# Kernel optimization log

Hardware: AMD Instinct MI355X
Metric: run time of the kernel (lower is better)

Reference implementation:

```python
import jax, jax.numpy as jnp
import numpy as np


def dct2_mat(N):
    # Orthonormal DCT-II matrix M[k, n]; scipy dct(norm='ortho') == M @ x,
    # and since M is orthogonal, idct(norm='ortho') == M.T @ x.
    n = jnp.arange(N, dtype=jnp.float32)
    k = jnp.arange(N, dtype=jnp.float32)[:, None]
    M = jnp.cos(jnp.pi * (n + 0.5) * k / N)
    scale = jnp.where(k == 0, jnp.sqrt(1.0 / N), jnp.sqrt(2.0 / N))
    return (M * scale).astype(jnp.float32)


def setup_inputs() -> dict:
    key = jax.random.key(0)
    x = jax.random.normal(key, (8, 32, 64, 64, 64), dtype=jnp.float32)
    return {"x": x}


def reference(x):
    # Faithful to original: DCT is applied along B, D, H (axes 0,1,2 of the
    # permuted [B,D,H,W,C] tensor), crop/pad acts on D,H,W, then IDCT along B,D,H.
    OUT = (32, 32, 32)
    TR = (32, 32, 32)
    B, C, D, H, W = x.shape
    CB, CD, CH = dct2_mat(B), dct2_mat(D), dct2_mat(H)

    # forward DCT-II (ortho) along B, D, H as batched matmuls
    y = jnp.einsum('kb,bcdhw->kcdhw', CB, x)
    y = jnp.einsum('kd,bcdhw->bckhw', CD, y)
    y = jnp.einsum('kh,bcdhw->bcdkw', CH, y)

    # spectral crop along D, H, W, then zero-pad up to output_size
    y = y[:, :, :TR[0], :TR[1], :TR[2]]
    y = jnp.pad(y, ((0, 0), (0, 0),
                    (0, OUT[0] - TR[0]),
                    (0, OUT[1] - TR[1]),
                    (0, OUT[2] - TR[2])))

    # inverse DCT (ortho) = transpose of the (orthogonal) DCT matrix
    Bi, Di, Hi = y.shape[0], y.shape[2], y.shape[3]
    z = jnp.einsum('kn,kcdhw->ncdhw', dct2_mat(Bi), y)
    z = jnp.einsum('kn,bckhw->bcnhw', dct2_mat(Di), z)
    z = jnp.einsum('kn,bcdkw->bcdnw', dct2_mat(Hi), z)
    return z
```

## Files before the change

### kernel.cpp

```cpp
#include <hip/hip_runtime.h>


constexpr double kPI = 3.14159265358979323846;

constexpr double cos_poly(double x) {
  double r = 1.0;
  for (int k = 15; k >= 1; --k) r = 1.0 - r * x * x / ((2.0 * k) * (2.0 * k - 1.0));
  return r;
}
constexpr double csqrt(double v) {
  double r = (v > 1.0) ? v : 1.0;
  for (int i = 0; i < 64; ++i) r = 0.5 * (r + v / r);
  return r;
}

struct C64T  { double c[128]; };
struct C128T { double c[256]; };
constexpr C64T make_c64() {
  C64T t{};
  for (int m = 0; m < 128; ++m) {
    int mm = (m > 64) ? m - 128 : m;
    t.c[m] = cos_poly(kPI * (double)mm / 64.0);
  }
  return t;
}
constexpr C128T make_c128() {
  C128T t{};
  for (int m = 0; m < 256; ++m) {
    int mm = (m > 128) ? m - 256 : m;
    t.c[m] = cos_poly(kPI * (double)mm / 128.0);
  }
  return t;
}
constexpr C64T  C64_  = make_c64();
constexpr C128T C128_ = make_c128();

struct ATabH { float a[16 * 64]; };
constexpr ATabH make_A_half(int n0) {
  ATabH t{};
  const double s32a = csqrt(1.0 / 32.0), s32b = csqrt(2.0 / 32.0);
  const double s64a = csqrt(1.0 / 64.0), s64b = csqrt(2.0 / 64.0);
  for (int ni = 0; ni < 16; ++ni)
    for (int h = 0; h < 64; ++h) {
      const int n = n0 + ni;
      double s = 0.0;
      for (int k = 0; k < 32; ++k) {
        double sc = ((k == 0) ? s32a : s32b) * ((k == 0) ? s64a : s64b);
        s += sc * C64_.c[((2 * n + 1) * k) % 128] * C128_.c[((2 * h + 1) * k) % 256];
      }
      t.a[ni * 64 + h] = (float)s;
    }
  return t;
}
constexpr ATabH A_LO = make_A_half(0);
constexpr ATabH A_HI = make_A_half(16);

__host__ __device__ constexpr float Aval(int n, int h) {
  return (n < 16) ? A_LO.a[n * 64 + h] : A_HI.a[(n - 16) * 64 + h];
}

struct AT2Tab { float a[8 * 64 * 4]; };
constexpr AT2Tab make_AT2() {
  AT2Tab t{};
  for (int ndg = 0; ndg < 8; ++ndg)
    for (int dg = 0; dg < 64; ++dg)
      for (int i = 0; i < 4; ++i)
        t.a[(ndg * 64 + dg) * 4 + i] = Aval(ndg * 4 + i, dg);
  return t;
}
__device__ const AT2Tab AT2_DEV = make_AT2();

template <int HB>
__device__ __forceinline__ void s1_group(float (&p)[32], const float (&xr)[16]) {
#pragma unroll
  for (int nh = 0; nh < 32; ++nh) {
    float s = p[nh];
#pragma unroll
    for (int i = 0; i < 16; ++i) s = fmaf(Aval(nh, HB + i), xr[i], s);
    p[nh] = s;
  }
}

__global__ __launch_bounds__(1024, 4) void spectral_kernel(
    const float* __restrict__ x, float* __restrict__ out) {
  __shared__ float V[32][32][33];

  const int tid = threadIdx.x;
  const int bc = blockIdx.x;
  const int wv = tid >> 6;
  const int dloc = tid >> 5;
  const int w = tid & 31;
  const int nhq = (tid >> 4) & 3;
  const int w16 = tid & 15;
  const int ndg = wv & 7;
  const int jg = wv >> 3;

  const float* xb = x + (size_t)bc * 262144;

  float acc[4][4][2];
#pragma unroll
  for (int i = 0; i < 4; ++i)
#pragma unroll
    for (int j = 0; j < 4; ++j) {
      acc[i][j][0] = 0.f;
      acc[i][j][1] = 0.f;
    }

#pragma unroll 1
  for (int cc = 0; cc < 2; ++cc) {
    const int d = cc * 32 + dloc;
    const float* xcol = xb + (size_t)d * 4096 + w;

    float p[32];
#pragma unroll
    for (int nh = 0; nh < 32; ++nh) p[nh] = 0.f;

    float xa[16], xc[16];
#pragma unroll
    for (int i = 0; i < 16; ++i) xa[i] = xcol[i * 64];
#pragma unroll
    for (int i = 0; i < 16; ++i) xc[i] = xcol[(16 + i) * 64];
    s1_group<0>(p, xa);
#pragma unroll
    for (int i = 0; i < 16; ++i) xa[i] = xcol[(32 + i) * 64];
    s1_group<16>(p, xc);
#pragma unroll
    for (int i = 0; i < 16; ++i) xc[i] = xcol[(48 + i) * 64];
    s1_group<32>(p, xa);
    s1_group<48>(p, xc);

#pragma unroll
    for (int nh = 0; nh < 32; ++nh) V[dloc][nh][w] = p[nh];
    __syncthreads();

    const float4* at4 = (const float4*)(AT2_DEV.a) + ndg * 64 + cc * 32;
#pragma unroll 8
    for (int dd = 0; dd < 32; ++dd) {
      const float4 a4 = at4[dd];
#pragma unroll
      for (int j = 0; j < 4; ++j) {
        const int nh = (jg * 4 + j) * 4 + nhq;
        const float2 v = *(const float2*)&V[dd][nh][w16 * 2];
        acc[0][j][0] = fmaf(a4.x, v.x, acc[0][j][0]);
        acc[0][j][1] = fmaf(a4.x, v.y, acc[0][j][1]);
        acc[1][j][0] = fmaf(a4.y, v.x, acc[1][j][0]);
        acc[1][j][1] = fmaf(a4.y, v.y, acc[1][j][1]);
        acc[2][j][0] = fmaf(a4.z, v.x, acc[2][j][0]);
        acc[2][j][1] = fmaf(a4.z, v.y, acc[2][j][1]);
        acc[3][j][0] = fmaf(a4.w, v.x, acc[3][j][0]);
        acc[3][j][1] = fmaf(a4.w, v.y, acc[3][j][1]);
      }
    }
    __syncthreads();
  }

  float* ob = out + (size_t)bc * 32768;
#pragma unroll
  for (int i = 0; i < 4; ++i) {
    const int nd = ndg * 4 + i;
#pragma unroll
    for (int j = 0; j < 4; ++j) {
      const int nh = (jg * 4 + j) * 4 + nhq;
      float2 v;
      v.x = acc[i][j][0];
      v.y = acc[i][j][1];
      *(float2*)(ob + nd * 1024 + nh * 32 + w16 * 2) = v;
    }
  }
}

extern "C" void kernel_launch(void* const* d_in, const int* in_sizes, int n_in,
                              void* d_out, int out_size, void* d_ws, size_t ws_size,
                              hipStream_t stream) {
  const float* x = (const float*)d_in[0];
  spectral_kernel<<<256, 1024, 0, stream>>>(x, (float*)d_out);
}
```

Before: 343.9 us.

## Split W across two blocks, prefetch next D-chunk, repad shared tile

Splits each (b,c) slab across two blocks by halving the W range, so the launch becomes 512 blocks of 512 threads instead of 256 of 1024. Each block uses a smaller shared buffer with custom strides chosen to avoid bank conflicts. The loads of the second D chunk are issued right after the first sync, overlapping memory latency with the stage-2 FMAs, and the final sync is dropped. The cost is that global accesses per wave become narrower (16-float rows), and holding the prefetched values raises register pressure.

```diff
diff --git a/kernel.cpp b/kernel.cpp
--- a/kernel.cpp
+++ b/kernel.cpp
@@ -81,21 +81,27 @@
   }
 }
 
-__global__ __launch_bounds__(1024, 4) void spectral_kernel(
+#define NH_STR 17
+#define D_STR  552
+
+__global__ __launch_bounds__(512, 4) void spectral_kernel(
     const float* __restrict__ x, float* __restrict__ out) {
-  __shared__ float V[32][32][33];
+  __shared__ float VS[32 * D_STR];
 
   const int tid = threadIdx.x;
-  const int bc = blockIdx.x;
+  const int bid = blockIdx.x;
+  const int bc = bid & 255;
+  const int whalf = bid >> 8;
+
   const int wv = tid >> 6;
-  const int dloc = tid >> 5;
-  const int w = tid & 31;
-  const int nhq = (tid >> 4) & 3;
-  const int w16 = tid & 15;
-  const int ndg = wv & 7;
-  const int jg = wv >> 3;
+  const int dloc = tid >> 4;
+  const int w = tid & 15;
+  const int l = tid & 63;
+  const int w8 = l & 7;
+  const int nhq = (l >> 3) & 3;
+  const int jg = l >> 5;
 
-  const float* xb = x + (size_t)bc * 262144;
+  const float* xb = x + (size_t)bc * 262144 + (whalf << 4);
 
   float acc[4][4][2];
 #pragma unroll
@@ -106,20 +112,23 @@
       acc[i][j][1] = 0.f;
     }
 
+  float xa[16], xc[16];
+  {
+    const float* xcol = xb + (size_t)dloc * 4096 + w;
+#pragma unroll
+    for (int i = 0; i < 16; ++i) xa[i] = xcol[i * 64];
+#pragma unroll
+    for (int i = 0; i < 16; ++i) xc[i] = xcol[(16 + i) * 64];
+  }
+
 #pragma unroll 1
   for (int cc = 0; cc < 2; ++cc) {
-    const int d = cc * 32 + dloc;
-    const float* xcol = xb + (size_t)d * 4096 + w;
+    const float* xcol = xb + (size_t)(cc * 32 + dloc) * 4096 + w;
 
     float p[32];
 #pragma unroll
     for (int nh = 0; nh < 32; ++nh) p[nh] = 0.f;
 
-    float xa[16], xc[16];
-#pragma unroll
-    for (int i = 0; i < 16; ++i) xa[i] = xcol[i * 64];
-#pragma unroll
-    for (int i = 0; i < 16; ++i) xc[i] = xcol[(16 + i) * 64];
     s1_group<0>(p, xa);
 #pragma unroll
     for (int i = 0; i < 16; ++i) xa[i] = xcol[(32 + i) * 64];
@@ -130,17 +139,26 @@
     s1_group<48>(p, xc);
 
 #pragma unroll
-    for (int nh = 0; nh < 32; ++nh) V[dloc][nh][w] = p[nh];
+    for (int nh = 0; nh < 32; ++nh) VS[dloc * D_STR + nh * NH_STR + w] = p[nh];
     __syncthreads();
 
-    const float4* at4 = (const float4*)(AT2_DEV.a) + ndg * 64 + cc * 32;
+    if (cc == 0) {
+      const float* xn = xb + (size_t)(32 + dloc) * 4096 + w;
+#pragma unroll
+      for (int i = 0; i < 16; ++i) xa[i] = xn[i * 64];
+#pragma unroll
+      for (int i = 0; i < 16; ++i) xc[i] = xn[(16 + i) * 64];
+    }
+
+    const float4* at4 = (const float4*)(AT2_DEV.a) + wv * 64 + cc * 32;
 #pragma unroll 8
     for (int dd = 0; dd < 32; ++dd) {
       const float4 a4 = at4[dd];
 #pragma unroll
       for (int j = 0; j < 4; ++j) {
-        const int nh = (jg * 4 + j) * 4 + nhq;
-        const float2 v = *(const float2*)&V[dd][nh][w16 * 2];
+        const int nh = jg * 16 + j * 4 + nhq;
+        const float2 v =
+            *(const float2*)&VS[dd * D_STR + nh * NH_STR + w8 * 2];
         acc[0][j][0] = fmaf(a4.x, v.x, acc[0][j][0]);
         acc[0][j][1] = fmaf(a4.x, v.y, acc[0][j][1]);
         acc[1][j][0] = fmaf(a4.y, v.x, acc[1][j][0]);
@@ -151,20 +169,20 @@
         acc[3][j][1] = fmaf(a4.w, v.y, acc[3][j][1]);
       }
     }
-    __syncthreads();
+    if (cc == 0) __syncthreads();
   }
 
-  float* ob = out + (size_t)bc * 32768;
+  float* ob = out + (size_t)bc * 32768 + (whalf << 4);
 #pragma unroll
   for (int i = 0; i < 4; ++i) {
-    const int nd = ndg * 4 + i;
+    const int nd = wv * 4 + i;
 #pragma unroll
     for (int j = 0; j < 4; ++j) {
-      const int nh = (jg * 4 + j) * 4 + nhq;
+      const int nh = jg * 16 + j * 4 + nhq;
       float2 v;
       v.x = acc[i][j][0];
       v.y = acc[i][j][1];
-      *(float2*)(ob + nd * 1024 + nh * 32 + w16 * 2) = v;
+      *(float2*)(ob + nd * 1024 + nh * 32 + w8 * 2) = v;
     }
   }
 }
@@ -173,5 +191,5 @@
                               void* d_out, int out_size, void* d_ws, size_t ws_size,
                               hipStream_t stream) {
   const float* x = (const float*)d_in[0];
-  spectral_kernel<<<256, 1024, 0, stream>>>(x, (float*)d_out);
+  spectral_kernel<<<512, 512, 0, stream>>>(x, (float*)d_out);
 }
```

Result: slower. 362.2 us (+5.3%).
